# Optimization experiments

Hardware: AMD Instinct MI355X
Metric: run time of the kernel (lower is better)

Reference implementation:

```python
import jax, jax.numpy as jnp
import numpy as np

N_NODES = 100000
N_EDGES = 1600000
N_GRAPHS = 512
IN_DIM = 128
HID = 128
N_CLASSES = 10


def _gcn_conv(x, W, b, src, dst, n):
    """PyG GCNConv: out = D^{-1/2} (A+I) D^{-1/2} (x @ W) + b."""
    xw = x @ W  # [n, out_dim]
    loop = jnp.arange(n)
    s = jnp.concatenate([src, loop])  # add self loops
    d = jnp.concatenate([dst, loop])
    deg = jax.ops.segment_sum(jnp.ones(s.shape, dtype=xw.dtype), d, num_segments=n)
    dinv = jnp.where(deg > 0, jax.lax.rsqrt(deg), jnp.zeros((), xw.dtype))
    norm = dinv[s] * dinv[d]  # [E + n]
    out = jax.ops.segment_sum(xw[s] * norm[:, None], d, num_segments=n)
    return out + b


def _global_mean_pool(x, batch, num_graphs):
    sums = jax.ops.segment_sum(x, batch, num_segments=num_graphs)
    cnts = jax.ops.segment_sum(jnp.ones(batch.shape, dtype=x.dtype), batch, num_segments=num_graphs)
    return sums / jnp.maximum(cnts, 1.0)[:, None]


def setup_inputs() -> dict:
    key = jax.random.key(0)
    ks = jax.random.split(key, 8)
    x = jax.random.normal(ks[0], (N_NODES, IN_DIM), dtype=jnp.float32)
    edge_index = jax.random.randint(ks[1], (2, N_EDGES), 0, N_NODES, dtype=jnp.int64)
    batch = jnp.sort(jax.random.randint(ks[2], (N_NODES,), 0, N_GRAPHS, dtype=jnp.int64))
    sc = 1.0 / np.sqrt(IN_DIM)
    W1 = jax.random.normal(ks[3], (IN_DIM, HID), dtype=jnp.float32) * sc
    b1 = jnp.zeros((HID,), dtype=jnp.float32)
    W2 = jax.random.normal(ks[4], (HID, HID), dtype=jnp.float32) * (1.0 / np.sqrt(HID))
    b2 = jnp.zeros((HID,), dtype=jnp.float32)
    Wc = jax.random.normal(ks[5], (HID, N_CLASSES), dtype=jnp.float32) * (1.0 / np.sqrt(HID))
    bc = jnp.zeros((N_CLASSES,), dtype=jnp.float32)
    return {"x": x, "edge_index": edge_index, "batch": batch,
            "W1": W1, "b1": b1, "W2": W2, "b2": b2, "Wc": Wc, "bc": bc}


def reference(x, edge_index, batch, W1, b1, W2, b2, Wc, bc):
    src, dst = edge_index[0], edge_index[1]
    n = x.shape[0]
    h = _gcn_conv(x, W1, b1, src, dst, n)
    h = jax.nn.relu(h)
    h = _gcn_conv(h, W2, b2, src, dst, n)
    g = _global_mean_pool(h, batch, N_GRAPHS)
    return g @ Wc + bc
```

## Files before the change

kernel.cpp:

```cpp
#include <hip/hip_runtime.h>

#define N_NODES 100000
#define N_EDGES 1600000
#define N_GRAPHS 512
#define DIM 128
#define NCLS 10
#define NBKT 782
#define BCAP 2560

typedef __attribute__((ext_vector_type(8))) short short8;
typedef __attribute__((ext_vector_type(4))) float f32x4;

static __device__ __forceinline__ unsigned short f2bf(float f) {
    unsigned u = __float_as_uint(f);
    unsigned r = (u + 0x7FFF + ((u >> 16) & 1)) >> 16;
    return (unsigned short)r;
}
static __device__ __forceinline__ float bf2f(unsigned u) {
    return __uint_as_float(u << 16);
}


__global__ void k_wprep(const float* __restrict__ W1, const float* __restrict__ W2,
                        unsigned short* __restrict__ wf1, unsigned short* __restrict__ wf2,
                        int* __restrict__ bcnt) {
    int b = blockIdx.x;
    if (b >= 128) {
        int i = (b - 128) * 256 + threadIdx.x;
        if (i < NBKT) bcnt[i] = 0;
        return;
    }
    const float* W = (b < 64) ? W1 : W2;
    unsigned short* wfrag = (b < 64) ? wf1 : wf2;
    int t = (b & 63) * 256 + threadIdx.x;
    int j = t & 7, lane = (t >> 3) & 63, nt = (t >> 9) & 7, kit = t >> 12;
    int k = kit * 32 + (lane >> 4) * 8 + j;
    int n = nt * 16 + (lane & 15);
    float v = W[k * 128 + n];
    unsigned short h = f2bf(v);
    wfrag[t] = h;
    wfrag[16384 + t] = f2bf(v - bf2f(h));
}


__global__ __launch_bounds__(256) void k_bucket(
    const int* __restrict__ src, const int* __restrict__ dst,
    int* __restrict__ bcnt, unsigned* __restrict__ bpack, int E) {
    __shared__ int cnt[NBKT];
    __shared__ int base[NBKT];
    int tid = threadIdx.x;
    for (int i = tid; i < NBKT; i += 256) cnt[i] = 0;
    __syncthreads();
    int e0 = blockIdx.x * 4096 + tid;
    unsigned pk[16]; short bk[16];
#pragma unroll
    for (int j = 0; j < 16; j++) {
        int e = e0 + j * 256;
        if (e < E) {
            int s = src[e], d = dst[e];
            bk[j] = (short)(d >> 7);
            pk[j] = ((unsigned)(d & 127) << 17) | (unsigned)s;
            atomicAdd(&cnt[bk[j]], 1);
        } else bk[j] = -1;
    }
    __syncthreads();
    for (int i = tid; i < NBKT; i += 256) {
        int c = cnt[i];
        base[i] = c ? atomicAdd(&bcnt[i], c) : 0;
        cnt[i] = 0;
    }
    __syncthreads();
#pragma unroll
    for (int j = 0; j < 16; j++) {
        if (bk[j] >= 0) {
            int p = base[bk[j]] + atomicAdd(&cnt[bk[j]], 1);
            if (p < BCAP) bpack[(size_t)bk[j] * BCAP + p] = pk[j];
        }
    }
}


__global__ __launch_bounds__(256) void k_bsort(
    const unsigned* __restrict__ bpack, const int* __restrict__ bcnt,
    int* __restrict__ rp, float* __restrict__ dinv,
    int* __restrict__ esrc, int N) {
    __shared__ int lds[256];
    __shared__ int gbase_sh;
    __shared__ int cnt[128];
    __shared__ int scan[128];
    __shared__ int cur[128];
    int b = blockIdx.x, tid = threadIdx.x;
    int v[4], pre[4];
    int s = 0;
#pragma unroll
    for (int j = 0; j < 4; j++) {
        int idx = tid * 4 + j;
        v[j] = (idx < NBKT) ? min(bcnt[idx], BCAP) : 0;
        pre[j] = s; s += v[j];
    }
    lds[tid] = s;
    __syncthreads();
    for (int off = 1; off < 256; off <<= 1) {
        int t = (tid >= off) ? lds[tid - off] : 0;
        __syncthreads();
        lds[tid] += t;
        __syncthreads();
    }
    if (tid == (b >> 2)) gbase_sh = lds[tid] - s + pre[b & 3];
    if (tid < 128) cnt[tid] = 0;
    __syncthreads();
    int gbase = gbase_sh;
    int n0 = b << 7;
    int m = min(bcnt[b], BCAP);
    const unsigned* bp = bpack + (size_t)b * BCAP;
    for (int j = tid; j < m; j += 256) atomicAdd(&cnt[bp[j] >> 17], 1);
    __syncthreads();
    if (tid < 128) scan[tid] = cnt[tid];
    __syncthreads();
    for (int off = 1; off < 128; off <<= 1) {
        int t = (tid < 128 && tid >= off) ? scan[tid - off] : 0;
        __syncthreads();
        if (tid < 128) scan[tid] += t;
        __syncthreads();
    }
    if (tid < 128) {
        int c = cnt[tid];
        int excl = scan[tid] - c;
        int node = n0 + tid;
        if (node <= N) rp[node] = gbase + excl;
        if (node < N) dinv[node] = rsqrtf((float)(c + 1));
        cur[tid] = gbase + excl;
    }
    __syncthreads();
    for (int j = tid; j < m; j += 256) {
        unsigned pk = bp[j];
        int p = atomicAdd(&cur[pk >> 17], 1);
        esrc[p] = (int)(pk & 0x1FFFF);
    }
}


__global__ __launch_bounds__(256) void k_gemm_f32(
    const float* __restrict__ A, const unsigned short* __restrict__ wfrag,
    const float* __restrict__ dinv, unsigned short* __restrict__ ybf, int M) {
    __shared__ unsigned short ldsw[4 * 32 * 136];
    int tid = threadIdx.x, wave = tid >> 6, lane = tid & 63;
    int m = lane & 15, quad = lane >> 4;
    int rowBase = blockIdx.x * 128 + wave * 32;
    int r0 = rowBase + m, r1 = rowBase + 16 + m;
    for (int i = tid; i < 2048; i += 256)
        ((short8*)ldsw)[i] = ((const short8*)wfrag)[i];
    __syncthreads();
    f32x4 acc0[8], acc1[8];
#pragma unroll
    for (int i = 0; i < 8; i++) { acc0[i] = (f32x4){0,0,0,0}; acc1[i] = (f32x4){0,0,0,0}; }
    const unsigned short* wlo = wfrag + 16384;

#pragma unroll
    for (int kit = 0; kit < 4; kit++) {
        float a0[8], a1[8];
        if (r0 < M) {
            const float4* ap = (const float4*)(A + (size_t)r0 * 128 + kit * 32 + quad * 8);
            float4 f0 = ap[0], f1 = ap[1];
            a0[0]=f0.x; a0[1]=f0.y; a0[2]=f0.z; a0[3]=f0.w; a0[4]=f1.x; a0[5]=f1.y; a0[6]=f1.z; a0[7]=f1.w;
        } else { for (int j = 0; j < 8; j++) a0[j] = 0.f; }
        if (r1 < M) {
            const float4* ap = (const float4*)(A + (size_t)r1 * 128 + kit * 32 + quad * 8);
            float4 f0 = ap[0], f1 = ap[1];
            a1[0]=f0.x; a1[1]=f0.y; a1[2]=f0.z; a1[3]=f0.w; a1[4]=f1.x; a1[5]=f1.y; a1[6]=f1.z; a1[7]=f1.w;
        } else { for (int j = 0; j < 8; j++) a1[j] = 0.f; }
        short8 ahi0, alo0, ahi1, alo1;
#pragma unroll
        for (int j = 0; j < 8; j++) {
            unsigned short h0 = f2bf(a0[j]);
            ahi0[j] = (short)h0; alo0[j] = (short)f2bf(a0[j] - bf2f(h0));
            unsigned short h1 = f2bf(a1[j]);
            ahi1[j] = (short)h1; alo1[j] = (short)f2bf(a1[j] - bf2f(h1));
        }
        int fb = kit * 4096 + lane * 8;
#pragma unroll
        for (int nt = 0; nt < 8; nt++) {
            int idx = fb + nt * 512;
            short8 bhi = *(const short8*)(ldsw + idx);
            short8 blo = *(const short8*)(wlo + idx);
            acc0[nt] = __builtin_amdgcn_mfma_f32_16x16x32_bf16(ahi0, bhi, acc0[nt], 0, 0, 0);
            acc0[nt] = __builtin_amdgcn_mfma_f32_16x16x32_bf16(alo0, bhi, acc0[nt], 0, 0, 0);
            acc0[nt] = __builtin_amdgcn_mfma_f32_16x16x32_bf16(ahi0, blo, acc0[nt], 0, 0, 0);
            acc1[nt] = __builtin_amdgcn_mfma_f32_16x16x32_bf16(ahi1, bhi, acc1[nt], 0, 0, 0);
            acc1[nt] = __builtin_amdgcn_mfma_f32_16x16x32_bf16(alo1, bhi, acc1[nt], 0, 0, 0);
            acc1[nt] = __builtin_amdgcn_mfma_f32_16x16x32_bf16(ahi1, blo, acc1[nt], 0, 0, 0);
        }
    }
    __syncthreads();
    float dv0 = (r0 < M) ? dinv[r0] : 0.f;
    float dv1 = (r1 < M) ? dinv[r1] : 0.f;
    unsigned short* wsm = ldsw + wave * 32 * 136;
#pragma unroll
    for (int rg = 0; rg < 4; rg++) {
        float s0 = __shfl(dv0, quad * 4 + rg);
        float s1 = __shfl(dv1, quad * 4 + rg);
#pragma unroll
        for (int nt = 0; nt < 8; nt++) {
            wsm[(quad * 4 + rg) * 136 + nt * 16 + m] = f2bf(acc0[nt][rg] * s0);
            wsm[(16 + quad * 4 + rg) * 136 + nt * 16 + m] = f2bf(acc1[nt][rg] * s1);
        }
    }
    __syncthreads();
#pragma unroll
    for (int i = 0; i < 8; i++) {
        int rl = i * 4 + quad;
        int grow = rowBase + rl;
        if (grow < M) {
            short8 v = *(const short8*)(wsm + rl * 136 + m * 8);
            *(short8*)(ybf + (size_t)grow * 128 + m * 8) = v;
        }
    }
}


__global__ __launch_bounds__(256) void k_gemm_bf(
    const unsigned short* __restrict__ A, const unsigned short* __restrict__ wfrag,
    const float* __restrict__ dinv, unsigned short* __restrict__ ybf, int M) {
    __shared__ unsigned short ldsw[4 * 32 * 136];
    int tid = threadIdx.x, wave = tid >> 6, lane = tid & 63;
    int m = lane & 15, quad = lane >> 4;
    int rowBase = blockIdx.x * 128 + wave * 32;
    int r0 = rowBase + m, r1 = rowBase + 16 + m;
    for (int i = tid; i < 2048; i += 256)
        ((short8*)ldsw)[i] = ((const short8*)wfrag)[i];
    __syncthreads();
    f32x4 acc0[8], acc1[8];
#pragma unroll
    for (int i = 0; i < 8; i++) { acc0[i] = (f32x4){0,0,0,0}; acc1[i] = (f32x4){0,0,0,0}; }
    const unsigned short* wlo = wfrag + 16384;

#pragma unroll
    for (int kit = 0; kit < 4; kit++) {
        short8 ah0, ah1;
        if (r0 < M) ah0 = *(const short8*)(A + (size_t)r0 * 128 + kit * 32 + quad * 8);
        else { for (int j = 0; j < 8; j++) ah0[j] = 0; }
        if (r1 < M) ah1 = *(const short8*)(A + (size_t)r1 * 128 + kit * 32 + quad * 8);
        else { for (int j = 0; j < 8; j++) ah1[j] = 0; }
        int fb = kit * 4096 + lane * 8;
#pragma unroll
        for (int nt = 0; nt < 8; nt++) {
            int idx = fb + nt * 512;
            short8 bhi = *(const short8*)(ldsw + idx);
            short8 blo = *(const short8*)(wlo + idx);
            acc0[nt] = __builtin_amdgcn_mfma_f32_16x16x32_bf16(ah0, bhi, acc0[nt], 0, 0, 0);
            acc0[nt] = __builtin_amdgcn_mfma_f32_16x16x32_bf16(ah0, blo, acc0[nt], 0, 0, 0);
            acc1[nt] = __builtin_amdgcn_mfma_f32_16x16x32_bf16(ah1, bhi, acc1[nt], 0, 0, 0);
            acc1[nt] = __builtin_amdgcn_mfma_f32_16x16x32_bf16(ah1, blo, acc1[nt], 0, 0, 0);
        }
    }
    __syncthreads();
    float dv0 = (r0 < M) ? dinv[r0] : 0.f;
    float dv1 = (r1 < M) ? dinv[r1] : 0.f;
    unsigned short* wsm = ldsw + wave * 32 * 136;
#pragma unroll
    for (int rg = 0; rg < 4; rg++) {
        float s0 = __shfl(dv0, quad * 4 + rg);
        float s1 = __shfl(dv1, quad * 4 + rg);
#pragma unroll
        for (int nt = 0; nt < 8; nt++) {
            wsm[(quad * 4 + rg) * 136 + nt * 16 + m] = f2bf(acc0[nt][rg] * s0);
            wsm[(16 + quad * 4 + rg) * 136 + nt * 16 + m] = f2bf(acc1[nt][rg] * s1);
        }
    }
    __syncthreads();
#pragma unroll
    for (int i = 0; i < 8; i++) {
        int rl = i * 4 + quad;
        int grow = rowBase + rl;
        if (grow < M) {
            short8 v = *(const short8*)(wsm + rl * 136 + m * 8);
            *(short8*)(ybf + (size_t)grow * 128 + m * 8) = v;
        }
    }
}


__global__ __launch_bounds__(256) void k_agg(
    const unsigned short* __restrict__ y, const float* __restrict__ dinv,
    const int* __restrict__ rp, const int* __restrict__ esrc,
    const float* __restrict__ bias, unsigned* __restrict__ out, int relu, int N) {
    int wave = threadIdx.x >> 6;
    int lane = threadIdx.x & 63;
    int node = blockIdx.x * 4 + wave;
    if (node >= N) return;
    const unsigned* y2 = (const unsigned*)y;
    unsigned vs = y2[(size_t)node * 64 + lane];
    float a0 = bf2f(vs & 0xFFFF), a1 = bf2f(vs >> 16);
    int beg = rp[node], end = rp[node + 1];
    int j = beg;
    while (j < end) {
        int idxv = (j + lane < end) ? esrc[j + lane] : 0;
        int cnt = end - j; if (cnt > 64) cnt = 64;
        int i = 0;
        for (; i + 4 <= cnt; i += 4) {
            int s0 = __shfl(idxv, i + 0);
            int s1 = __shfl(idxv, i + 1);
            int s2 = __shfl(idxv, i + 2);
            int s3 = __shfl(idxv, i + 3);
            unsigned v0 = y2[(size_t)s0 * 64 + lane];
            unsigned v1 = y2[(size_t)s1 * 64 + lane];
            unsigned v2 = y2[(size_t)s2 * 64 + lane];
            unsigned v3 = y2[(size_t)s3 * 64 + lane];
            a0 += bf2f(v0 & 0xFFFF); a1 += bf2f(v0 >> 16);
            a0 += bf2f(v1 & 0xFFFF); a1 += bf2f(v1 >> 16);
            a0 += bf2f(v2 & 0xFFFF); a1 += bf2f(v2 >> 16);
            a0 += bf2f(v3 & 0xFFFF); a1 += bf2f(v3 >> 16);
        }
        for (; i < cnt; i++) {
            int s = __shfl(idxv, i);
            unsigned v = y2[(size_t)s * 64 + lane];
            a0 += bf2f(v & 0xFFFF); a1 += bf2f(v >> 16);
        }
        j += cnt;
    }
    float s = dinv[node];
    float2 bv = ((const float2*)bias)[lane];
    float o0 = s * a0 + bv.x;
    float o1 = s * a1 + bv.y;
    if (relu) { o0 = fmaxf(o0, 0.f); o1 = fmaxf(o1, 0.f); }
    out[(size_t)node * 64 + lane] = (unsigned)f2bf(o0) | ((unsigned)f2bf(o1) << 16);
}


__global__ __launch_bounds__(256) void k_poolhead(
    const unsigned* __restrict__ h2, const int* __restrict__ batch,
    const float* __restrict__ Wc, const float* __restrict__ bc,
    float* __restrict__ out, int n) {
    __shared__ float2 red[4][64];
    __shared__ float grow[DIM];
    int gid = blockIdx.x;
    int tid = threadIdx.x, wave = tid >> 6, lane = tid & 63;
    int lo = 0, hi = n;
    while (lo < hi) { int mid = (lo + hi) >> 1; if (batch[mid] < gid) lo = mid + 1; else hi = mid; }
    int start = lo;
    hi = n;
    while (lo < hi) { int mid = (lo + hi) >> 1; if (batch[mid] < gid + 1) lo = mid + 1; else hi = mid; }
    int end = lo;
    float a0 = 0.f, a1 = 0.f;
    for (int r = start + wave; r < end; r += 4) {
        unsigned v = h2[(size_t)r * 64 + lane];
        a0 += bf2f(v & 0xFFFF); a1 += bf2f(v >> 16);
    }
    red[wave][lane] = make_float2(a0, a1);
    __syncthreads();
    if (tid < 64) {
        float2 s = red[0][tid];
        s.x += red[1][tid].x; s.y += red[1][tid].y;
        s.x += red[2][tid].x; s.y += red[2][tid].y;
        s.x += red[3][tid].x; s.y += red[3][tid].y;
        int cnt = end - start;
        float inv = 1.f / (float)(cnt > 0 ? cnt : 1);
        grow[tid * 2] = s.x * inv;
        grow[tid * 2 + 1] = s.y * inv;
    }
    __syncthreads();
    if (tid < NCLS) {
        float acc = bc[tid];
#pragma unroll 16
        for (int k = 0; k < DIM; k++) acc += grow[k] * Wc[k * NCLS + tid];
        out[gid * NCLS + tid] = acc;
    }
}

extern "C" void kernel_launch(void* const* d_in, const int* in_sizes, int n_in,
                              void* d_out, int out_size, void* d_ws, size_t ws_size,
                              hipStream_t stream) {
    const float* x    = (const float*)d_in[0];
    const int*   ei   = (const int*)d_in[1];
    const int*   batch= (const int*)d_in[2];
    const float* W1   = (const float*)d_in[3];
    const float* b1   = (const float*)d_in[4];
    const float* W2   = (const float*)d_in[5];
    const float* b2   = (const float*)d_in[6];
    const float* Wc   = (const float*)d_in[7];
    const float* bc   = (const float*)d_in[8];
    float* out = (float*)d_out;
    const int N = N_NODES, E = N_EDGES;
    const int* src = ei;
    const int* dst = ei + E;

    char* ws = (char*)d_ws;
    size_t off = 0;
    auto carve = [&](size_t bytes) -> void* {
        void* p = ws + off;
        off = (off + bytes + 255) & ~(size_t)255;
        return p;
    };
    int*      rp    = (int*)     carve((size_t)(N + 1) * 4);
    float*    dinv  = (float*)   carve((size_t)N * 4);
    int*      bcnt  = (int*)     carve(NBKT * 4);
    unsigned* bpack = (unsigned*)carve((size_t)NBKT * BCAP * 4);
    int*      esrc  = (int*)     carve((size_t)E * 4);
    unsigned short* wf1 = (unsigned short*)carve(2 * 16384 * 2);
    unsigned short* wf2 = (unsigned short*)carve(2 * 16384 * 2);
    unsigned short* bufY = (unsigned short*)carve((size_t)N * DIM * 2);
    unsigned short* bufH = (unsigned short*)carve((size_t)N * DIM * 2);
    (void)ws_size; (void)n_in; (void)in_sizes; (void)out_size;

    hipLaunchKernelGGL(k_wprep,  dim3(128 + (NBKT + 255) / 256), dim3(256), 0, stream, W1, W2, wf1, wf2, bcnt);
    hipLaunchKernelGGL(k_bucket, dim3((E + 4095) / 4096), dim3(256), 0, stream, src, dst, bcnt, bpack, E);
    hipLaunchKernelGGL(k_bsort,  dim3(NBKT), dim3(256), 0, stream, bpack, bcnt, rp, dinv, esrc, N);

    int gemmGrid = (N + 127) / 128;
    hipLaunchKernelGGL(k_gemm_f32, dim3(gemmGrid), dim3(256), 0, stream, x, wf1, dinv, bufY, N);
    hipLaunchKernelGGL(k_agg, dim3((N + 3) / 4), dim3(256), 0, stream, bufY, dinv, rp, esrc, b1, (unsigned*)bufH, 1, N);
    hipLaunchKernelGGL(k_gemm_bf, dim3(gemmGrid), dim3(256), 0, stream, bufH, wf2, dinv, bufY, N);
    hipLaunchKernelGGL(k_agg, dim3((N + 3) / 4), dim3(256), 0, stream, bufY, dinv, rp, esrc, b2, (unsigned*)bufH, 0, N);
    hipLaunchKernelGGL(k_poolhead, dim3(N_GRAPHS), dim3(256), 0, stream, (const unsigned*)bufH, batch, Wc, bc, out, N);
}
```

Before: 343.3 us.

## Use coarser 1024-node dst buckets for CSR build with 1024-thread sort blocks

Changes the two-pass bucketed CSR construction from 782 buckets of 128 destination nodes to 98 buckets of 1024 nodes. Each sort block now uses 1024 threads and scans 1024 node counts, while bucketing blocks handle 2048 edges each. The aim is less global-atomic contention spread and fewer, fuller bucket/sort blocks. The trade-off is only 98 sort blocks, which may underfill the GPU, heavier LDS atomic contention per bucket, and longer 1024-wide scans.

```diff
diff --git a/kernel.cpp b/kernel.cpp
--- a/kernel.cpp
+++ b/kernel.cpp
@@ -5,8 +5,8 @@
 #define N_GRAPHS 512
 #define DIM 128
 #define NCLS 10
-#define NBKT 782
-#define BCAP 2560
+#define NBKT 98
+#define BCAP 17408
 
 typedef __attribute__((ext_vector_type(8))) short short8;
 typedef __attribute__((ext_vector_type(4))) float f32x4;
@@ -26,7 +26,7 @@
                         int* __restrict__ bcnt) {
     int b = blockIdx.x;
     if (b >= 128) {
-        int i = (b - 128) * 256 + threadIdx.x;
+        int i = threadIdx.x;
         if (i < NBKT) bcnt[i] = 0;
         return;
     }
@@ -49,29 +49,29 @@
     __shared__ int cnt[NBKT];
     __shared__ int base[NBKT];
     int tid = threadIdx.x;
-    for (int i = tid; i < NBKT; i += 256) cnt[i] = 0;
-    __syncthreads();
-    int e0 = blockIdx.x * 4096 + tid;
-    unsigned pk[16]; short bk[16];
-#pragma unroll
-    for (int j = 0; j < 16; j++) {
+    if (tid < NBKT) cnt[tid] = 0;
+    __syncthreads();
+    int e0 = blockIdx.x * 2048 + tid;
+    unsigned pk[8]; short bk[8];
+#pragma unroll
+    for (int j = 0; j < 8; j++) {
         int e = e0 + j * 256;
         if (e < E) {
             int s = src[e], d = dst[e];
-            bk[j] = (short)(d >> 7);
-            pk[j] = ((unsigned)(d & 127) << 17) | (unsigned)s;
+            bk[j] = (short)(d >> 10);
+            pk[j] = ((unsigned)(d & 1023) << 17) | (unsigned)s;
             atomicAdd(&cnt[bk[j]], 1);
         } else bk[j] = -1;
     }
     __syncthreads();
-    for (int i = tid; i < NBKT; i += 256) {
-        int c = cnt[i];
-        base[i] = c ? atomicAdd(&bcnt[i], c) : 0;
-        cnt[i] = 0;
-    }
-    __syncthreads();
-#pragma unroll
-    for (int j = 0; j < 16; j++) {
+    if (tid < NBKT) {
+        int c = cnt[tid];
+        base[tid] = c ? atomicAdd(&bcnt[tid], c) : 0;
+        cnt[tid] = 0;
+    }
+    __syncthreads();
+#pragma unroll
+    for (int j = 0; j < 8; j++) {
         if (bk[j] >= 0) {
             int p = base[bk[j]] + atomicAdd(&cnt[bk[j]], 1);
             if (p < BCAP) bpack[(size_t)bk[j] * BCAP + p] = pk[j];
@@ -80,59 +80,46 @@
 }
 
 
-__global__ __launch_bounds__(256) void k_bsort(
+__global__ __launch_bounds__(1024) void k_bsort(
     const unsigned* __restrict__ bpack, const int* __restrict__ bcnt,
     int* __restrict__ rp, float* __restrict__ dinv,
     int* __restrict__ esrc, int N) {
-    __shared__ int lds[256];
-    __shared__ int gbase_sh;
-    __shared__ int cnt[128];
-    __shared__ int scan[128];
-    __shared__ int cur[128];
+    __shared__ int csum[128];
+    __shared__ int cnt[1024];
+    __shared__ int scan[1024];
+    __shared__ int cur[1024];
     int b = blockIdx.x, tid = threadIdx.x;
-    int v[4], pre[4];
-    int s = 0;
-#pragma unroll
-    for (int j = 0; j < 4; j++) {
-        int idx = tid * 4 + j;
-        v[j] = (idx < NBKT) ? min(bcnt[idx], BCAP) : 0;
-        pre[j] = s; s += v[j];
-    }
-    lds[tid] = s;
-    __syncthreads();
-    for (int off = 1; off < 256; off <<= 1) {
-        int t = (tid >= off) ? lds[tid - off] : 0;
+    if (tid < 128) csum[tid] = (tid < NBKT) ? min(bcnt[tid], BCAP) : 0;
+    cnt[tid] = 0;
+    __syncthreads();
+    for (int off = 1; off < 128; off <<= 1) {
+        int t = (tid < 128 && tid >= off) ? csum[tid - off] : 0;
         __syncthreads();
-        lds[tid] += t;
+        if (tid < 128) csum[tid] += t;
         __syncthreads();
     }
-    if (tid == (b >> 2)) gbase_sh = lds[tid] - s + pre[b & 3];
-    if (tid < 128) cnt[tid] = 0;
-    __syncthreads();
-    int gbase = gbase_sh;
-    int n0 = b << 7;
+    int gbase = (b == 0) ? 0 : csum[b - 1];
     int m = min(bcnt[b], BCAP);
+    int n0 = b << 10;
     const unsigned* bp = bpack + (size_t)b * BCAP;
-    for (int j = tid; j < m; j += 256) atomicAdd(&cnt[bp[j] >> 17], 1);
-    __syncthreads();
-    if (tid < 128) scan[tid] = cnt[tid];
-    __syncthreads();
-    for (int off = 1; off < 128; off <<= 1) {
-        int t = (tid < 128 && tid >= off) ? scan[tid - off] : 0;
+    for (int j = tid; j < m; j += 1024) atomicAdd(&cnt[bp[j] >> 17], 1);
+    __syncthreads();
+    scan[tid] = cnt[tid];
+    __syncthreads();
+    for (int off = 1; off < 1024; off <<= 1) {
+        int t = (tid >= off) ? scan[tid - off] : 0;
         __syncthreads();
-        if (tid < 128) scan[tid] += t;
+        scan[tid] += t;
         __syncthreads();
     }
-    if (tid < 128) {
-        int c = cnt[tid];
-        int excl = scan[tid] - c;
-        int node = n0 + tid;
-        if (node <= N) rp[node] = gbase + excl;
-        if (node < N) dinv[node] = rsqrtf((float)(c + 1));
-        cur[tid] = gbase + excl;
-    }
-    __syncthreads();
-    for (int j = tid; j < m; j += 256) {
+    int c = cnt[tid];
+    int excl = scan[tid] - c;
+    int node = n0 + tid;
+    if (node <= N) rp[node] = gbase + excl;
+    if (node < N) dinv[node] = rsqrtf((float)(c + 1));
+    cur[tid] = gbase + excl;
+    __syncthreads();
+    for (int j = tid; j < m; j += 1024) {
         unsigned pk = bp[j];
         int p = atomicAdd(&cur[pk >> 17], 1);
         esrc[p] = (int)(pk & 0x1FFFF);
@@ -402,9 +389,9 @@
     unsigned short* bufH = (unsigned short*)carve((size_t)N * DIM * 2);
     (void)ws_size; (void)n_in; (void)in_sizes; (void)out_size;
 
-    hipLaunchKernelGGL(k_wprep,  dim3(128 + (NBKT + 255) / 256), dim3(256), 0, stream, W1, W2, wf1, wf2, bcnt);
-    hipLaunchKernelGGL(k_bucket, dim3((E + 4095) / 4096), dim3(256), 0, stream, src, dst, bcnt, bpack, E);
-    hipLaunchKernelGGL(k_bsort,  dim3(NBKT), dim3(256), 0, stream, bpack, bcnt, rp, dinv, esrc, N);
+    hipLaunchKernelGGL(k_wprep,  dim3(129), dim3(256), 0, stream, W1, W2, wf1, wf2, bcnt);
+    hipLaunchKernelGGL(k_bucket, dim3((E + 2047) / 2048), dim3(256), 0, stream, src, dst, bcnt, bpack, E);
+    hipLaunchKernelGGL(k_bsort,  dim3(NBKT), dim3(1024), 0, stream, bpack, bcnt, rp, dinv, esrc, N);
 
     int gemmGrid = (N + 127) / 128;
     hipLaunchKernelGGL(k_gemm_f32, dim3(gemmGrid), dim3(256), 0, stream, x, wf1, dinv, bufY, N);
```

Result: no change. 347.1 us (+1.1%).

## Process four nodes per wavefront in aggregation with 16-byte gathers

Applied to the files above, without the earlier changes.

The aggregation kernel now splits each 64-lane wavefront into four 16-lane groups, each handling one destination node, and loads neighbour rows as 16-byte uint4 vectors instead of 4-byte words. Each lane accumulates eight features. The aim is fewer, wider memory transactions per gathered row and more independent rows in flight per wave. The trade-off is that every group in a wave loops to the largest degree among its four nodes, so uneven degrees leave lanes idle. The grid is now N/16 with no bounds check, which relies on N being a multiple of 16.

```diff
diff --git a/kernel.cpp b/kernel.cpp
--- a/kernel.cpp
+++ b/kernel.cpp
@@ -284,46 +284,53 @@
     const unsigned short* __restrict__ y, const float* __restrict__ dinv,
     const int* __restrict__ rp, const int* __restrict__ esrc,
     const float* __restrict__ bias, unsigned* __restrict__ out, int relu, int N) {
+    int lane = threadIdx.x & 63;
     int wave = threadIdx.x >> 6;
-    int lane = threadIdx.x & 63;
-    int node = blockIdx.x * 4 + wave;
-    if (node >= N) return;
-    const unsigned* y2 = (const unsigned*)y;
-    unsigned vs = y2[(size_t)node * 64 + lane];
-    float a0 = bf2f(vs & 0xFFFF), a1 = bf2f(vs >> 16);
+    int g = lane >> 4;
+    int s = lane & 15;
+    int node = (blockIdx.x * 4 + wave) * 4 + g;
+    const uint4* y4 = (const uint4*)y;
     int beg = rp[node], end = rp[node + 1];
-    int j = beg;
-    while (j < end) {
-        int idxv = (j + lane < end) ? esrc[j + lane] : 0;
-        int cnt = end - j; if (cnt > 64) cnt = 64;
-        int i = 0;
-        for (; i + 4 <= cnt; i += 4) {
-            int s0 = __shfl(idxv, i + 0);
-            int s1 = __shfl(idxv, i + 1);
-            int s2 = __shfl(idxv, i + 2);
-            int s3 = __shfl(idxv, i + 3);
-            unsigned v0 = y2[(size_t)s0 * 64 + lane];
-            unsigned v1 = y2[(size_t)s1 * 64 + lane];
-            unsigned v2 = y2[(size_t)s2 * 64 + lane];
-            unsigned v3 = y2[(size_t)s3 * 64 + lane];
-            a0 += bf2f(v0 & 0xFFFF); a1 += bf2f(v0 >> 16);
-            a0 += bf2f(v1 & 0xFFFF); a1 += bf2f(v1 >> 16);
-            a0 += bf2f(v2 & 0xFFFF); a1 += bf2f(v2 >> 16);
-            a0 += bf2f(v3 & 0xFFFF); a1 += bf2f(v3 >> 16);
-        }
-        for (; i < cnt; i++) {
-            int s = __shfl(idxv, i);
-            unsigned v = y2[(size_t)s * 64 + lane];
-            a0 += bf2f(v & 0xFFFF); a1 += bf2f(v >> 16);
-        }
-        j += cnt;
-    }
-    float s = dinv[node];
-    float2 bv = ((const float2*)bias)[lane];
-    float o0 = s * a0 + bv.x;
-    float o1 = s * a1 + bv.y;
-    if (relu) { o0 = fmaxf(o0, 0.f); o1 = fmaxf(o1, 0.f); }
-    out[(size_t)node * 64 + lane] = (unsigned)f2bf(o0) | ((unsigned)f2bf(o1) << 16);
+    int cnt = end - beg;
+    int mc = max(cnt, __shfl_xor(cnt, 16));
+    mc = max(mc, __shfl_xor(mc, 32));
+    uint4 v0 = y4[(size_t)node * 16 + s];
+    float a0 = bf2f(v0.x & 0xFFFF), a1 = bf2f(v0.x >> 16);
+    float a2 = bf2f(v0.y & 0xFFFF), a3 = bf2f(v0.y >> 16);
+    float a4 = bf2f(v0.z & 0xFFFF), a5 = bf2f(v0.z >> 16);
+    float a6 = bf2f(v0.w & 0xFFFF), a7 = bf2f(v0.w >> 16);
+    int idxchunk = 0;
+    for (int i = 0; i < mc; i++) {
+        if ((i & 15) == 0) {
+            int p = beg + i + s;
+            idxchunk = esrc[(p < end) ? p : beg];
+        }
+        int idx = __shfl(idxchunk, (lane & 48) + (i & 15));
+        if (i < cnt) {
+            uint4 v = y4[(size_t)idx * 16 + s];
+            a0 += bf2f(v.x & 0xFFFF); a1 += bf2f(v.x >> 16);
+            a2 += bf2f(v.y & 0xFFFF); a3 += bf2f(v.y >> 16);
+            a4 += bf2f(v.z & 0xFFFF); a5 += bf2f(v.z >> 16);
+            a6 += bf2f(v.w & 0xFFFF); a7 += bf2f(v.w >> 16);
+        }
+    }
+    float dv = dinv[node];
+    float4 b0 = ((const float4*)bias)[s * 2];
+    float4 b1 = ((const float4*)bias)[s * 2 + 1];
+    float o0 = dv * a0 + b0.x, o1 = dv * a1 + b0.y;
+    float o2 = dv * a2 + b0.z, o3 = dv * a3 + b0.w;
+    float o4 = dv * a4 + b1.x, o5 = dv * a5 + b1.y;
+    float o6 = dv * a6 + b1.z, o7 = dv * a7 + b1.w;
+    if (relu) {
+        o0 = fmaxf(o0, 0.f); o1 = fmaxf(o1, 0.f); o2 = fmaxf(o2, 0.f); o3 = fmaxf(o3, 0.f);
+        o4 = fmaxf(o4, 0.f); o5 = fmaxf(o5, 0.f); o6 = fmaxf(o6, 0.f); o7 = fmaxf(o7, 0.f);
+    }
+    uint4 ov;
+    ov.x = (unsigned)f2bf(o0) | ((unsigned)f2bf(o1) << 16);
+    ov.y = (unsigned)f2bf(o2) | ((unsigned)f2bf(o3) << 16);
+    ov.z = (unsigned)f2bf(o4) | ((unsigned)f2bf(o5) << 16);
+    ov.w = (unsigned)f2bf(o6) | ((unsigned)f2bf(o7) << 16);
+    ((uint4*)out)[(size_t)node * 16 + s] = ov;
 }
 
 
@@ -407,9 +414,10 @@
     hipLaunchKernelGGL(k_bsort,  dim3(NBKT), dim3(256), 0, stream, bpack, bcnt, rp, dinv, esrc, N);
 
     int gemmGrid = (N + 127) / 128;
+    int aggGrid = N / 16;
     hipLaunchKernelGGL(k_gemm_f32, dim3(gemmGrid), dim3(256), 0, stream, x, wf1, dinv, bufY, N);
-    hipLaunchKernelGGL(k_agg, dim3((N + 3) / 4), dim3(256), 0, stream, bufY, dinv, rp, esrc, b1, (unsigned*)bufH, 1, N);
+    hipLaunchKernelGGL(k_agg, dim3(aggGrid), dim3(256), 0, stream, bufY, dinv, rp, esrc, b1, (unsigned*)bufH, 1, N);
     hipLaunchKernelGGL(k_gemm_bf, dim3(gemmGrid), dim3(256), 0, stream, bufH, wf2, dinv, bufY, N);
-    hipLaunchKernelGGL(k_agg, dim3((N + 3) / 4), dim3(256), 0, stream, bufY, dinv, rp, esrc, b2, (unsigned*)bufH, 0, N);
+    hipLaunchKernelGGL(k_agg, dim3(aggGrid), dim3(256), 0, stream, bufY, dinv, rp, esrc, b2, (unsigned*)bufH, 0, N);
     hipLaunchKernelGGL(k_poolhead, dim3(N_GRAPHS), dim3(256), 0, stream, (const unsigned*)bufH, batch, Wc, bc, out, N);
 }
```

New measurement: 347.7 us. Within noise of the previous version (+1.3%).
